# Optimization experiments

Measured on AMD Instinct MI355X. Metric: run time of the kernel, lower is better.

The kernel has to match this reference:

```python
import jax, jax.numpy as jnp
import numpy as np

D_MODEL = 512
D_STATE = 32
EXPAND = 2
D_INNER = D_MODEL * EXPAND
BATCH = 2
SEQ_LEN = 1024


def setup_inputs() -> dict:
    key = jax.random.key(0)
    ks = jax.random.split(key, 8)
    s = lambda fan_in: 1.0 / np.sqrt(fan_in)
    x = jax.random.normal(ks[0], (BATCH, SEQ_LEN, D_MODEL), dtype=jnp.float32)
    Wx = jax.random.uniform(ks[1], (D_INNER, D_MODEL), minval=-s(D_MODEL), maxval=s(D_MODEL))
    Wdt = jax.random.uniform(ks[2], (D_INNER, D_MODEL), minval=-s(D_MODEL), maxval=s(D_MODEL))
    bdt = jax.random.uniform(ks[3], (D_INNER,)) + 1.0  # dt_proj.bias init: rand + 1
    A_log = jnp.log(jax.random.uniform(ks[4], (D_INNER, D_STATE), minval=1e-4, maxval=1.0))
    WB = jax.random.uniform(ks[5], (D_INNER * D_STATE, D_MODEL), minval=-s(D_MODEL), maxval=s(D_MODEL))
    WC = jax.random.uniform(ks[6], (D_INNER * D_STATE, D_MODEL), minval=-s(D_MODEL), maxval=s(D_MODEL))
    Wout = jax.random.uniform(ks[7], (D_MODEL, D_INNER), minval=-s(D_INNER), maxval=s(D_INNER))
    return {"x": x, "Wx": Wx, "Wdt": Wdt, "bdt": bdt, "A_log": A_log,
            "WB": WB, "WC": WC, "Wout": Wout}


def reference(x, Wx, Wdt, bdt, A_log, WB, WC, Wout):
    b, L, _ = x.shape
    d_inner, d_state = A_log.shape

    x_inner = jnp.einsum('bld,ed->ble', x, Wx)                 # (b, L, d_inner)
    delta = jax.nn.softplus(jnp.einsum('bld,ed->ble', x, Wdt) + bdt)
    A = -jnp.exp(A_log.astype(jnp.float32))                    # (d_inner, d_state)
    A_disc = jnp.exp(delta[..., None] * A)                     # (b, L, d_inner, d_state)
    Bm = jnp.einsum('bld,ed->ble', x, WB).reshape(b, L, d_inner, d_state)
    Cm = jnp.einsum('bld,ed->ble', x, WC).reshape(b, L, d_inner, d_state)

    def step(h, inp):
        a_t, b_t, c_t, x_t = inp
        h = a_t * h + b_t * x_t[..., None]                     # (b, d_inner, d_state)
        y = jnp.sum(c_t * h, axis=-1)                          # (b, d_inner)
        return h, y

    h0 = jnp.zeros((b, d_inner, d_state), dtype=x.dtype)
    xs = (jnp.moveaxis(A_disc, 1, 0), jnp.moveaxis(Bm, 1, 0),
          jnp.moveaxis(Cm, 1, 0), jnp.moveaxis(x_inner, 1, 0))
    _, ys = jax.lax.scan(step, h0, xs)                         # ys: (L, b, d_inner)
    y = jnp.moveaxis(ys, 0, 1)
    y = y * jax.nn.sigmoid(y)                                  # SiLU
    return jnp.einsum('ble,de->bld', y, Wout)
```

## Files before the change

### kernel.cpp

```cpp
#include <hip/hip_runtime.h>
#include <utility>

#define BATCH   2
#define SEQLEN  1024
#define DMODEL  512
#define DSTATE  32
#define DINNER  1024
#define MROWS   (BATCH*SEQLEN)
#define NPROJ   (2*DINNER + 2*DINNER*DSTATE)

typedef short bf16x8 __attribute__((ext_vector_type(8)));
typedef float f32x4  __attribute__((ext_vector_type(4)));

template <int... Is, class F>
__device__ __forceinline__ void static_for_impl(std::integer_sequence<int, Is...>, F&& f) {
    (f(std::integral_constant<int, Is>{}), ...);
}
template <int N, class F>
__device__ __forceinline__ void static_for(F&& f) {
    static_for_impl(std::make_integer_sequence<int, N>{}, static_cast<F&&>(f));
}

__device__ __forceinline__ unsigned short f2bf(float f) {
    union { float f; unsigned u; } c; c.f = f;
    unsigned u = c.u;
    u += 0x7fffu + ((u >> 16) & 1u);
    return (unsigned short)(u >> 16);
}
__device__ __forceinline__ float bf2f(unsigned short h) {
    union { unsigned u; float f; } c; c.u = ((unsigned)h) << 16;
    return c.f;
}

__global__ void cast_all(const float4* __restrict__ Wx, const float4* __restrict__ Wdt,
                         const float4* __restrict__ WB, const float4* __restrict__ WC,
                         const float4* __restrict__ x,  const float4* __restrict__ Wout,
                         unsigned short* __restrict__ Wbf,
                         unsigned short* __restrict__ Xbf,
                         unsigned short* __restrict__ Woutbf) {
    const long nWx = 131072, nWdt = 131072, nWB = 4194304, nWC = 4194304;
    const long nWall = nWx + nWdt + nWB + nWC;
    const long nX = 262144, nWo = 131072;
    const long total = nWall + nX + nWo;
    for (long u = (long)blockIdx.x * blockDim.x + threadIdx.x; u < total;
         u += (long)gridDim.x * blockDim.x) {
        float4 v; unsigned short* dst;
        if (u < nWall) {
            if (u < nWx)             v = Wx[u];
            else if (u < nWx+nWdt)   v = Wdt[u - nWx];
            else if (u < nWx+nWdt+nWB) v = WB[u - nWx - nWdt];
            else                     v = WC[u - nWx - nWdt - nWB];
            dst = Wbf + u*4;
        } else if (u < nWall + nX) {
            v = x[u - nWall];       dst = Xbf + (u - nWall)*4;
        } else {
            v = Wout[u - nWall - nX]; dst = Woutbf + (u - nWall - nX)*4;
        }
        ushort4 o; o.x = f2bf(v.x); o.y = f2bf(v.y); o.z = f2bf(v.z); o.w = f2bf(v.w);
        *(ushort4*)dst = o;
    }
}

template<int EPI, int KCT>
__global__ __launch_bounds__(256)
void gemm_bt(const unsigned short* __restrict__ A, const unsigned short* __restrict__ Bw,
             int N, int t0, int Tchunk, int tgs,
             unsigned short* __restrict__ xinb, float* __restrict__ dlt,
             unsigned short* __restrict__ Bout, unsigned short* __restrict__ Cout,
             const float* __restrict__ bdt, float* __restrict__ outf) {
    __shared__ unsigned short Asm[2][128*32];
    __shared__ unsigned short Bsm[2][128*32];
    constexpr int K  = KCT;
    constexpr int nt = KCT >> 5;
    const int tid  = threadIdx.x;
    const int w    = tid >> 6;
    const int lane = tid & 63;
    const int wm   = w >> 1, wn = w & 1;

    const int nx = gridDim.x, ny = gridDim.y;
    int ntile, rtile;
    if ((nx & 7) == 0) {
        const int lin = blockIdx.x + nx * blockIdx.y;
        const int xcd = lin & 7;
        const int sl  = lin >> 3;
        ntile = xcd * (nx >> 3) + sl / ny;
        rtile = sl % ny;
    } else {
        ntile = blockIdx.x; rtile = blockIdx.y;
    }

    const int rr0  = rtile * 128;
    const int bb   = (rr0 >= Tchunk) ? 1 : 0;
    const int grow0 = bb * SEQLEN + t0 + (rr0 - bb * Tchunk);
    const int n0   = ntile * 128;

    f32x4 acc[4][4] = {};

    const unsigned short* Ag = A  + (size_t)grow0 * K;
    const unsigned short* Bg = Bw + (size_t)n0 * K;

    const int c0 = w*64 + lane;
    const int c1 = c0 + 256;
    const int r   = lane & 15;
    const int h16 = lane >> 4;

    const int rowc0 = c0 >> 2, rowc1 = c1 >> 2;
    const int subc0 = (c0 & 3) ^ ((c0 >> 3) & 3);
    const int subc1 = (c1 & 3) ^ ((c1 >> 3) & 3);
    typedef const __attribute__((address_space(1))) unsigned short gq_t;
    gq_t* agp0 = (gq_t*)(Ag + (size_t)rowc0 * K + subc0 * 8);
    gq_t* agp1 = (gq_t*)(Ag + (size_t)rowc1 * K + subc1 * 8);
    gq_t* bgp0 = (gq_t*)(Bg + (size_t)rowc0 * K + subc0 * 8);
    gq_t* bgp1 = (gq_t*)(Bg + (size_t)rowc1 * K + subc1 * 8);

    #define STAGE(koff_, buf_)                                                            \
        do {                                                                              \
            __builtin_amdgcn_global_load_lds((const __attribute__((address_space(1))) void*)(agp0 + (koff_)), \
                (__attribute__((address_space(3))) void*)(&Asm[(buf_)][w*512]), 16, 0, 0);\
            __builtin_amdgcn_global_load_lds((const __attribute__((address_space(1))) void*)(agp1 + (koff_)), \
                (__attribute__((address_space(3))) void*)(&Asm[(buf_)][2048 + w*512]), 16, 0, 0); \
            __builtin_amdgcn_global_load_lds((const __attribute__((address_space(1))) void*)(bgp0 + (koff_)), \
                (__attribute__((address_space(3))) void*)(&Bsm[(buf_)][w*512]), 16, 0, 0);\
            __builtin_amdgcn_global_load_lds((const __attribute__((address_space(1))) void*)(bgp1 + (koff_)), \
                (__attribute__((address_space(3))) void*)(&Bsm[(buf_)][2048 + w*512]), 16, 0, 0); \
        } while (0)

    #define COMPUTE(buf_)                                                                 \
        do {                                                                              \
            bf16x8 af[4], bfr[4];                                                         \
            _Pragma("unroll")                                                             \
            for (int i = 0; i < 4; i++) {                                                 \
                const int Ra = wm*64 + i*16 + r;                                          \
                const int Rb = wn*64 + i*16 + r;                                          \
                af[i]  = *(const bf16x8*)(&Asm[(buf_)][Ra*32 + (h16 ^ ((Ra>>1)&3))*8]);   \
                bfr[i] = *(const bf16x8*)(&Bsm[(buf_)][Rb*32 + (h16 ^ ((Rb>>1)&3))*8]);   \
            }                                                                             \
            _Pragma("unroll")                                                             \
            for (int i = 0; i < 4; i++)                                                   \
                _Pragma("unroll")                                                         \
                for (int j = 0; j < 4; j++)                                               \
                    acc[i][j] = __builtin_amdgcn_mfma_f32_16x16x32_bf16(af[i], bfr[j], acc[i][j], 0, 0, 0); \
        } while (0)

    STAGE(0, 0);
    static_for<nt - 1>([&](auto itc) {
        constexpr int it  = decltype(itc)::value;
        constexpr int cur = it & 1;
        STAGE((it + 1) * 32, cur ^ 1);
        asm volatile("s_waitcnt vmcnt(4)" ::: "memory");
        __builtin_amdgcn_s_barrier();
        COMPUTE(cur);
        asm volatile("" ::: "memory");
        __builtin_amdgcn_s_barrier();
        asm volatile("" ::: "memory");
    });
    asm volatile("s_waitcnt vmcnt(0)" ::: "memory");
    __builtin_amdgcn_s_barrier();
    {
        constexpr int last = (nt - 1) & 1;
        COMPUTE(last);
    }

    #undef STAGE
    #undef COMPUTE

    const int q = lane >> 4;
    const int Tg  = 1 << tgs;
    const int NT  = Tg >> 3;
    #pragma unroll
    for (int i = 0; i < 4; i++) {
        const int lr0 = wm*64 + i*16 + q*4;
        #pragma unroll
        for (int j = 0; j < 4; j++) {
            const int ncol = n0 + wn*64 + j*16 + r;
            if (EPI == 0) {
                const int cr   = rr0 + lr0;
                const int lt   = cr - bb*Tchunk;
                const int seg  = lt >> tgs;
                const int tloc = lt & (Tg - 1);
                const int kin  = tloc >> 3;
                const int tin  = tloc & 7;
                const int bs   = bb*8 + seg;
                if (ncol < 1024) {
                    short4 o;
                    o.x = (short)f2bf(acc[i][j][0]); o.y = (short)f2bf(acc[i][j][1]);
                    o.z = (short)f2bf(acc[i][j][2]); o.w = (short)f2bf(acc[i][j][3]);
                    *(short4*)(xinb + ((size_t)bs*1024 + ncol)*Tg + tloc) = o;
                } else if (ncol < 2048) {
                    const float bias = bdt[ncol - 1024];
                    float4 o;
                    {   float z0 = acc[i][j][0] + bias; o.x = (z0 > 20.f) ? z0 : log1pf(__expf(z0));
                        float z1 = acc[i][j][1] + bias; o.y = (z1 > 20.f) ? z1 : log1pf(__expf(z1));
                        float z2 = acc[i][j][2] + bias; o.z = (z2 > 20.f) ? z2 : log1pf(__expf(z2));
                        float z3 = acc[i][j][3] + bias; o.w = (z3 > 20.f) ? z3 : log1pf(__expf(z3)); }
                    *(float4*)(dlt + ((size_t)bs*1024 + (ncol-1024))*Tg + tloc) = o;
                } else if (ncol < 34816) {
                    const int es = ncol - 2048;
                    short4 o;
                    o.x = (short)f2bf(acc[i][j][0]); o.y = (short)f2bf(acc[i][j][1]);
                    o.z = (short)f2bf(acc[i][j][2]); o.w = (short)f2bf(acc[i][j][3]);
                    *(short4*)(Bout + (((size_t)bs*1024 + (es>>5))*NT + kin)*256 + (es&31)*8 + tin) = o;
                } else {
                    const int es = ncol - 34816;
                    short4 o;
                    o.x = (short)f2bf(acc[i][j][0]); o.y = (short)f2bf(acc[i][j][1]);
                    o.z = (short)f2bf(acc[i][j][2]); o.w = (short)f2bf(acc[i][j][3]);
                    *(short4*)(Cout + (((size_t)bs*1024 + (es>>5))*NT + kin)*256 + (es&31)*8 + tin) = o;
                }
            } else {
                #pragma unroll
                for (int t = 0; t < 4; t++)
                    outf[(size_t)(grow0 + lr0 + t)*N + ncol] = acc[i][j][t];
            }
        }
    }
}

template<int NT>
__global__ __launch_bounds__(256)
void scan_fused(const float* __restrict__ dlt, const unsigned short* __restrict__ xinb,
                const unsigned short* __restrict__ Bbf, const unsigned short* __restrict__ Cbf,
                const float* __restrict__ A_log,
                unsigned short* __restrict__ Ybf, float* __restrict__ hbuf,
                int t0, int first) {
    const int tid = threadIdx.x;
    const int g = tid >> 5, s = tid & 31;
    const int G = blockIdx.x;
    const int b = G >> 10, e = G & 1023;
    const int bs = b*8 + g;
    const int Tg = NT * 8;

    const float Aes = -__expf(A_log[e*32 + s]);

    const float*          dp = dlt  + ((size_t)bs*1024 + e)*Tg;
    const unsigned short* xp = xinb + ((size_t)bs*1024 + e)*Tg;
    const unsigned short* bp = Bbf  + ((size_t)bs*1024 + e)*NT*256 + s*8;
    const unsigned short* cp = Cbf  + ((size_t)bs*1024 + e)*NT*256 + s*8;

    const float hin0 = first ? 0.f : hbuf[(size_t)G*32 + s];

    float h = 0.f, ap = 1.f;
    #pragma unroll 2
    for (int k = 0; k < NT; k++) {
        const bf16x8 bv = *(const bf16x8*)(bp + (size_t)k*256);
        const bf16x8 xv = *(const bf16x8*)(xp + k*8);
        const float4 d0 = *(const float4*)(dp + k*8), d1 = *(const float4*)(dp + k*8 + 4);
        const float db[8] = {d0.x,d0.y,d0.z,d0.w,d1.x,d1.y,d1.z,d1.w};
        #pragma unroll
        for (int j = 0; j < 8; j++) {
            const float a = __expf(db[j] * Aes);
            h = a*h + bf2f((unsigned short)bv[j])*bf2f((unsigned short)xv[j]);
            ap *= a;
        }
    }

    __shared__ float Lh[8][32];
    __shared__ float La[8][32];
    Lh[g][s] = h; La[g][s] = ap;
    __syncthreads();
    float hin = hin0;
    #pragma unroll
    for (int j = 0; j < 7; j++) {
        if (j < g) hin = La[j][s]*hin + Lh[j][s];
    }
    if (g == 7) hbuf[(size_t)G*32 + s] = La[7][s]*hin + Lh[7][s];

    h = hin;
    const int tbase = t0 + g*Tg;
    #pragma unroll 2
    for (int k = 0; k < NT; k++) {
        const bf16x8 bv = *(const bf16x8*)(bp + (size_t)k*256);
        const bf16x8 cv = *(const bf16x8*)(cp + (size_t)k*256);
        const bf16x8 xv = *(const bf16x8*)(xp + k*8);
        const float4 d0 = *(const float4*)(dp + k*8), d1 = *(const float4*)(dp + k*8 + 4);
        const float db[8] = {d0.x,d0.y,d0.z,d0.w,d1.x,d1.y,d1.z,d1.w};
        float p[8];
        #pragma unroll
        for (int j = 0; j < 8; j++) {
            const float a = __expf(db[j] * Aes);
            h = a*h + bf2f((unsigned short)bv[j])*bf2f((unsigned short)xv[j]);
            p[j] = bf2f((unsigned short)cv[j])*h;
        }
        #pragma unroll
        for (int i2 = 0; i2 < 4; i2++) {
            float send = (s & 16) ? p[i2] : p[i2+4];
            float recv = __shfl_xor(send, 16, 32);
            p[i2] = ((s & 16) ? p[i2+4] : p[i2]) + recv;
        }
        #pragma unroll
        for (int i2 = 0; i2 < 2; i2++) {
            float send = (s & 8) ? p[i2] : p[i2+2];
            float recv = __shfl_xor(send, 8, 32);
            p[i2] = ((s & 8) ? p[i2+2] : p[i2]) + recv;
        }
        {
            float send = (s & 4) ? p[0] : p[1];
            float recv = __shfl_xor(send, 4, 32);
            p[0] = ((s & 4) ? p[1] : p[0]) + recv;
        }
        p[0] += __shfl_xor(p[0], 2, 32);
        p[0] += __shfl_xor(p[0], 1, 32);
        if ((s & 3) == 0) {
            const int tl = s >> 2;
            const float qv = p[0];
            const float y = qv * __builtin_amdgcn_rcpf(1.f + __expf(-qv));
            Ybf[(size_t)b*1048576 + e + (size_t)(tbase + k*8 + tl)*1024] = f2bf(y);
        }
    }
}

extern "C" void kernel_launch(void* const* d_in, const int* in_sizes, int n_in,
                              void* d_out, int out_size, void* d_ws, size_t ws_size,
                              hipStream_t stream) {
    const float* x     = (const float*)d_in[0];
    const float* Wx    = (const float*)d_in[1];
    const float* Wdt   = (const float*)d_in[2];
    const float* bdt   = (const float*)d_in[3];
    const float* A_log = (const float*)d_in[4];
    const float* WB    = (const float*)d_in[5];
    const float* WC    = (const float*)d_in[6];
    const float* Wout  = (const float*)d_in[7];

    char* ws = (char*)d_ws;
    unsigned short* Wbf    = (unsigned short*)(ws);
    unsigned short* Xbf    = (unsigned short*)(ws + 69206016);
    unsigned short* Woutbf = (unsigned short*)(ws + 71303168);
    unsigned short* xinb   = (unsigned short*)(ws + 72351744);
    float*          dlt    = (float*)        (ws + 76546048);
    unsigned short* Ybf    = (unsigned short*)(ws + 84934656);
    float*          hbuf   = (float*)        (ws + 89128960);
    unsigned short* Bbf    = (unsigned short*)(ws + 89391104);
    const size_t fixedB = 89391104;

    int T = 128;
    const int cands[4] = {1024, 512, 256, 128};
    for (int ci = 0; ci < 4; ci++) {
        if (fixedB + (size_t)2 * cands[ci] * 131072 <= ws_size) { T = cands[ci]; break; }
    }
    unsigned short* Cbf = Bbf + (size_t)T * 65536;

    const int Tg = T / 8;
    int tgs = 0; while ((1 << tgs) < Tg) tgs++;
    const int NT = Tg / 8;

    cast_all<<<dim3(2048), dim3(256), 0, stream>>>(
        (const float4*)Wx, (const float4*)Wdt, (const float4*)WB, (const float4*)WC,
        (const float4*)x, (const float4*)Wout, Wbf, Xbf, Woutbf);

    const int NC = SEQLEN / T;
    for (int c = 0; c < NC; c++) {
        const int t0 = c * T;
        const int first = (c == 0) ? 1 : 0;
        gemm_bt<0, DMODEL><<<dim3(NPROJ/128, 2*T/128), dim3(256), 0, stream>>>(
            Xbf, Wbf, NPROJ, t0, T, tgs, xinb, dlt, Bbf, Cbf, bdt, nullptr);
        if (NT == 16)
            scan_fused<16><<<dim3(2048), dim3(256), 0, stream>>>(
                dlt, xinb, Bbf, Cbf, A_log, Ybf, hbuf, t0, first);
        else if (NT == 8)
            scan_fused<8><<<dim3(2048), dim3(256), 0, stream>>>(
                dlt, xinb, Bbf, Cbf, A_log, Ybf, hbuf, t0, first);
        else if (NT == 4)
            scan_fused<4><<<dim3(2048), dim3(256), 0, stream>>>(
                dlt, xinb, Bbf, Cbf, A_log, Ybf, hbuf, t0, first);
        else
            scan_fused<2><<<dim3(2048), dim3(256), 0, stream>>>(
                dlt, xinb, Bbf, Cbf, A_log, Ybf, hbuf, t0, first);
    }

    gemm_bt<1, DINNER><<<dim3(DMODEL/128, MROWS/128), dim3(256), 0, stream>>>(
        Ybf, Woutbf, DMODEL, 0, MROWS, 0, nullptr, nullptr, nullptr, nullptr, nullptr,
        (float*)d_out);
}
```

Before: 357.6 us.

## Use 256x256 tiles with 512 threads for the projection GEMM

Splits the GEMM into a dedicated large-tile projection kernel (256x256 output tile, K-step 64, 8 waves, direct global-to-LDS loads) and a separate smaller output-projection kernel. The larger tile raises arithmetic intensity and data reuse for the dominant projection GEMM, which produces about 67K columns. The minimum chunk size rises to 256 rows so the row tile fits. The cost is higher LDS use (128KB) and register pressure, which may limit occupancy.

```diff
diff --git a/kernel.cpp b/kernel.cpp
--- a/kernel.cpp
+++ b/kernel.cpp
@@ -61,21 +61,21 @@
     }
 }
 
-template<int EPI, int KCT>
-__global__ __launch_bounds__(256)
-void gemm_bt(const unsigned short* __restrict__ A, const unsigned short* __restrict__ Bw,
-             int N, int t0, int Tchunk, int tgs,
+template<int KCT>
+__global__ __launch_bounds__(512, 2)
+void gemm256(const unsigned short* __restrict__ A, const unsigned short* __restrict__ Bw,
+             int t0, int Tchunk, int tgs,
              unsigned short* __restrict__ xinb, float* __restrict__ dlt,
              unsigned short* __restrict__ Bout, unsigned short* __restrict__ Cout,
-             const float* __restrict__ bdt, float* __restrict__ outf) {
-    __shared__ unsigned short Asm[2][128*32];
-    __shared__ unsigned short Bsm[2][128*32];
+             const float* __restrict__ bdt) {
+    __shared__ unsigned short Asm[2][256*64];
+    __shared__ unsigned short Bsm[2][256*64];
     constexpr int K  = KCT;
-    constexpr int nt = KCT >> 5;
+    constexpr int nt = KCT >> 6;
     const int tid  = threadIdx.x;
-    const int w    = tid >> 6;
+    const int wid  = tid >> 6;
     const int lane = tid & 63;
-    const int wm   = w >> 1, wn = w & 1;
+    const int wr   = wid >> 2, wc = wid & 3;
 
     const int nx = gridDim.x, ny = gridDim.y;
     int ntile, rtile;
@@ -89,10 +89,154 @@
         ntile = blockIdx.x; rtile = blockIdx.y;
     }
 
-    const int rr0  = rtile * 128;
+    const int rr0  = rtile * 256;
     const int bb   = (rr0 >= Tchunk) ? 1 : 0;
     const int grow0 = bb * SEQLEN + t0 + (rr0 - bb * Tchunk);
-    const int n0   = ntile * 128;
+    const int n0   = ntile * 256;
+
+    f32x4 acc[8][4] = {};
+
+    const unsigned short* Ag = A  + (size_t)grow0 * K;
+    const unsigned short* Bg = Bw + (size_t)n0 * K;
+
+    const int r   = lane & 15;
+    const int h16 = lane >> 4;
+
+    typedef const __attribute__((address_space(1))) unsigned short gq_t;
+    const int cqA = tid;
+    const int cq0 = cqA, cq1 = cqA + 512, cq2 = cqA + 1024, cq3 = cqA + 1536;
+    const size_t so0 = (size_t)(cq0 >> 3) * K + ((cq0 & 7) ^ ((cq0 >> 3) & 7)) * 8;
+    const size_t so1 = (size_t)(cq1 >> 3) * K + ((cq1 & 7) ^ ((cq1 >> 3) & 7)) * 8;
+    const size_t so2 = (size_t)(cq2 >> 3) * K + ((cq2 & 7) ^ ((cq2 >> 3) & 7)) * 8;
+    const size_t so3 = (size_t)(cq3 >> 3) * K + ((cq3 & 7) ^ ((cq3 >> 3) & 7)) * 8;
+    gq_t* ag = (gq_t*)Ag;
+    gq_t* bg = (gq_t*)Bg;
+
+    #define GLDS(srcp_, dsto_, buf_, mat_)                                                \
+        __builtin_amdgcn_global_load_lds((const __attribute__((address_space(1))) void*)(srcp_), \
+            (__attribute__((address_space(3))) void*)(&mat_[(buf_)][(dsto_)]), 16, 0, 0)
+
+    #define STAGE(koff_, buf_)                                                            \
+        do {                                                                              \
+            GLDS(ag + so0 + (koff_), tid*8,         buf_, Asm);                           \
+            GLDS(ag + so1 + (koff_), tid*8 + 4096,  buf_, Asm);                           \
+            GLDS(ag + so2 + (koff_), tid*8 + 8192,  buf_, Asm);                           \
+            GLDS(ag + so3 + (koff_), tid*8 + 12288, buf_, Asm);                           \
+            GLDS(bg + so0 + (koff_), tid*8,         buf_, Bsm);                           \
+            GLDS(bg + so1 + (koff_), tid*8 + 4096,  buf_, Bsm);                           \
+            GLDS(bg + so2 + (koff_), tid*8 + 8192,  buf_, Bsm);                           \
+            GLDS(bg + so3 + (koff_), tid*8 + 12288, buf_, Bsm);                           \
+        } while (0)
+
+    #define COMPUTE(buf_)                                                                 \
+        do {                                                                              \
+            _Pragma("unroll")                                                             \
+            for (int kk = 0; kk < 2; kk++) {                                              \
+                bf16x8 af[8], bfr[4];                                                     \
+                _Pragma("unroll")                                                         \
+                for (int i = 0; i < 8; i++) {                                             \
+                    const int Ra = wr*128 + i*16 + r;                                     \
+                    const int sa = (kk*4 + h16) ^ (Ra & 7);                               \
+                    af[i] = *(const bf16x8*)(&Asm[(buf_)][Ra*64 + sa*8]);                 \
+                }                                                                         \
+                _Pragma("unroll")                                                         \
+                for (int j = 0; j < 4; j++) {                                             \
+                    const int Rb = wc*64 + j*16 + r;                                      \
+                    const int sb = (kk*4 + h16) ^ (Rb & 7);                               \
+                    bfr[j] = *(const bf16x8*)(&Bsm[(buf_)][Rb*64 + sb*8]);                \
+                }                                                                         \
+                _Pragma("unroll")                                                         \
+                for (int i = 0; i < 8; i++)                                               \
+                    _Pragma("unroll")                                                     \
+                    for (int j = 0; j < 4; j++)                                           \
+                        acc[i][j] = __builtin_amdgcn_mfma_f32_16x16x32_bf16(af[i], bfr[j], acc[i][j], 0, 0, 0); \
+            }                                                                             \
+        } while (0)
+
+    STAGE(0, 0);
+    static_for<nt - 1>([&](auto itc) {
+        constexpr int it  = decltype(itc)::value;
+        constexpr int cur = it & 1;
+        STAGE((it + 1) * 64, cur ^ 1);
+        asm volatile("s_waitcnt vmcnt(8)" ::: "memory");
+        __builtin_amdgcn_s_barrier();
+        COMPUTE(cur);
+        asm volatile("" ::: "memory");
+        __builtin_amdgcn_s_barrier();
+        asm volatile("" ::: "memory");
+    });
+    asm volatile("s_waitcnt vmcnt(0)" ::: "memory");
+    __builtin_amdgcn_s_barrier();
+    {
+        constexpr int last = (nt - 1) & 1;
+        COMPUTE(last);
+    }
+
+    #undef STAGE
+    #undef COMPUTE
+    #undef GLDS
+
+    const int q = lane >> 4;
+    const int Tg  = 1 << tgs;
+    const int NT  = Tg >> 3;
+    #pragma unroll
+    for (int i = 0; i < 8; i++) {
+        const int lr0 = wr*128 + i*16 + q*4;
+        #pragma unroll
+        for (int j = 0; j < 4; j++) {
+            const int ncol = n0 + wc*64 + j*16 + r;
+            const int cr   = rr0 + lr0;
+            const int lt   = cr - bb*Tchunk;
+            const int seg  = lt >> tgs;
+            const int tloc = lt & (Tg - 1);
+            const int kin  = tloc >> 3;
+            const int tin  = tloc & 7;
+            const int bs   = bb*8 + seg;
+            if (ncol < 1024) {
+                short4 o;
+                o.x = (short)f2bf(acc[i][j][0]); o.y = (short)f2bf(acc[i][j][1]);
+                o.z = (short)f2bf(acc[i][j][2]); o.w = (short)f2bf(acc[i][j][3]);
+                *(short4*)(xinb + ((size_t)bs*1024 + ncol)*Tg + tloc) = o;
+            } else if (ncol < 2048) {
+                const float bias = bdt[ncol - 1024];
+                float4 o;
+                {   float z0 = acc[i][j][0] + bias; o.x = (z0 > 20.f) ? z0 : log1pf(__expf(z0));
+                    float z1 = acc[i][j][1] + bias; o.y = (z1 > 20.f) ? z1 : log1pf(__expf(z1));
+                    float z2 = acc[i][j][2] + bias; o.z = (z2 > 20.f) ? z2 : log1pf(__expf(z2));
+                    float z3 = acc[i][j][3] + bias; o.w = (z3 > 20.f) ? z3 : log1pf(__expf(z3)); }
+                *(float4*)(dlt + ((size_t)bs*1024 + (ncol-1024))*Tg + tloc) = o;
+            } else if (ncol < 34816) {
+                const int es = ncol - 2048;
+                short4 o;
+                o.x = (short)f2bf(acc[i][j][0]); o.y = (short)f2bf(acc[i][j][1]);
+                o.z = (short)f2bf(acc[i][j][2]); o.w = (short)f2bf(acc[i][j][3]);
+                *(short4*)(Bout + (((size_t)bs*1024 + (es>>5))*NT + kin)*256 + (es&31)*8 + tin) = o;
+            } else {
+                const int es = ncol - 34816;
+                short4 o;
+                o.x = (short)f2bf(acc[i][j][0]); o.y = (short)f2bf(acc[i][j][1]);
+                o.z = (short)f2bf(acc[i][j][2]); o.w = (short)f2bf(acc[i][j][3]);
+                *(short4*)(Cout + (((size_t)bs*1024 + (es>>5))*NT + kin)*256 + (es&31)*8 + tin) = o;
+            }
+        }
+    }
+}
+
+template<int KCT>
+__global__ __launch_bounds__(256)
+void gemm_out(const unsigned short* __restrict__ A, const unsigned short* __restrict__ Bw,
+              int N, float* __restrict__ outf) {
+    __shared__ unsigned short Asm[2][128*32];
+    __shared__ unsigned short Bsm[2][128*32];
+    constexpr int K  = KCT;
+    constexpr int nt = KCT >> 5;
+    const int tid  = threadIdx.x;
+    const int w    = tid >> 6;
+    const int lane = tid & 63;
+    const int wm   = w >> 1, wn = w & 1;
+
+    const int grow0 = blockIdx.y * 128;
+    const int n0    = blockIdx.x * 128;
 
     f32x4 acc[4][4] = {};
 
@@ -160,58 +304,19 @@
         constexpr int last = (nt - 1) & 1;
         COMPUTE(last);
     }
-
     #undef STAGE
     #undef COMPUTE
 
     const int q = lane >> 4;
-    const int Tg  = 1 << tgs;
-    const int NT  = Tg >> 3;
     #pragma unroll
     for (int i = 0; i < 4; i++) {
         const int lr0 = wm*64 + i*16 + q*4;
         #pragma unroll
         for (int j = 0; j < 4; j++) {
             const int ncol = n0 + wn*64 + j*16 + r;
-            if (EPI == 0) {
-                const int cr   = rr0 + lr0;
-                const int lt   = cr - bb*Tchunk;
-                const int seg  = lt >> tgs;
-                const int tloc = lt & (Tg - 1);
-                const int kin  = tloc >> 3;
-                const int tin  = tloc & 7;
-                const int bs   = bb*8 + seg;
-                if (ncol < 1024) {
-                    short4 o;
-                    o.x = (short)f2bf(acc[i][j][0]); o.y = (short)f2bf(acc[i][j][1]);
-                    o.z = (short)f2bf(acc[i][j][2]); o.w = (short)f2bf(acc[i][j][3]);
-                    *(short4*)(xinb + ((size_t)bs*1024 + ncol)*Tg + tloc) = o;
-                } else if (ncol < 2048) {
-                    const float bias = bdt[ncol - 1024];
-                    float4 o;
-                    {   float z0 = acc[i][j][0] + bias; o.x = (z0 > 20.f) ? z0 : log1pf(__expf(z0));
-                        float z1 = acc[i][j][1] + bias; o.y = (z1 > 20.f) ? z1 : log1pf(__expf(z1));
-                        float z2 = acc[i][j][2] + bias; o.z = (z2 > 20.f) ? z2 : log1pf(__expf(z2));
-                        float z3 = acc[i][j][3] + bias; o.w = (z3 > 20.f) ? z3 : log1pf(__expf(z3)); }
-                    *(float4*)(dlt + ((size_t)bs*1024 + (ncol-1024))*Tg + tloc) = o;
-                } else if (ncol < 34816) {
-                    const int es = ncol - 2048;
-                    short4 o;
-                    o.x = (short)f2bf(acc[i][j][0]); o.y = (short)f2bf(acc[i][j][1]);
-                    o.z = (short)f2bf(acc[i][j][2]); o.w = (short)f2bf(acc[i][j][3]);
-                    *(short4*)(Bout + (((size_t)bs*1024 + (es>>5))*NT + kin)*256 + (es&31)*8 + tin) = o;
-                } else {
-                    const int es = ncol - 34816;
-                    short4 o;
-                    o.x = (short)f2bf(acc[i][j][0]); o.y = (short)f2bf(acc[i][j][1]);
-                    o.z = (short)f2bf(acc[i][j][2]); o.w = (short)f2bf(acc[i][j][3]);
-                    *(short4*)(Cout + (((size_t)bs*1024 + (es>>5))*NT + kin)*256 + (es&31)*8 + tin) = o;
-                }
-            } else {
-                #pragma unroll
-                for (int t = 0; t < 4; t++)
-                    outf[(size_t)(grow0 + lr0 + t)*N + ncol] = acc[i][j][t];
-            }
+            #pragma unroll
+            for (int t = 0; t < 4; t++)
+                outf[(size_t)(grow0 + lr0 + t)*N + ncol] = acc[i][j][t];
         }
     }
 }
@@ -332,9 +437,9 @@
     unsigned short* Bbf    = (unsigned short*)(ws + 89391104);
     const size_t fixedB = 89391104;
 
-    int T = 128;
-    const int cands[4] = {1024, 512, 256, 128};
-    for (int ci = 0; ci < 4; ci++) {
+    int T = 256;
+    const int cands[3] = {1024, 512, 256};
+    for (int ci = 0; ci < 3; ci++) {
         if (fixedB + (size_t)2 * cands[ci] * 131072 <= ws_size) { T = cands[ci]; break; }
     }
     unsigned short* Cbf = Bbf + (size_t)T * 65536;
@@ -351,23 +456,19 @@
     for (int c = 0; c < NC; c++) {
         const int t0 = c * T;
         const int first = (c == 0) ? 1 : 0;
-        gemm_bt<0, DMODEL><<<dim3(NPROJ/128, 2*T/128), dim3(256), 0, stream>>>(
-            Xbf, Wbf, NPROJ, t0, T, tgs, xinb, dlt, Bbf, Cbf, bdt, nullptr);
+        gemm256<DMODEL><<<dim3(NPROJ/256, 2*T/256), dim3(512), 0, stream>>>(
+            Xbf, Wbf, t0, T, tgs, xinb, dlt, Bbf, Cbf, bdt);
         if (NT == 16)
             scan_fused<16><<<dim3(2048), dim3(256), 0, stream>>>(
                 dlt, xinb, Bbf, Cbf, A_log, Ybf, hbuf, t0, first);
         else if (NT == 8)
             scan_fused<8><<<dim3(2048), dim3(256), 0, stream>>>(
                 dlt, xinb, Bbf, Cbf, A_log, Ybf, hbuf, t0, first);
-        else if (NT == 4)
+        else
             scan_fused<4><<<dim3(2048), dim3(256), 0, stream>>>(
                 dlt, xinb, Bbf, Cbf, A_log, Ybf, hbuf, t0, first);
-        else
-            scan_fused<2><<<dim3(2048), dim3(256), 0, stream>>>(
-                dlt, xinb, Bbf, Cbf, A_log, Ybf, hbuf, t0, first);
-    }
-
-    gemm_bt<1, DINNER><<<dim3(DMODEL/128, MROWS/128), dim3(256), 0, stream>>>(
-        Ybf, Woutbf, DMODEL, 0, MROWS, 0, nullptr, nullptr, nullptr, nullptr, nullptr,
-        (float*)d_out);
-}
+    }
+
+    gemm_out<DINNER><<<dim3(DMODEL/128, MROWS/128), dim3(256), 0, stream>>>(
+        Ybf, Woutbf, DMODEL, (float*)d_out);
+}
```

Result: slower. 381.8 us (+6.8%).
